# Kernel optimization log

Measured on AMD Instinct MI355X. Metric: run time of the kernel, lower is better.

The kernel has to match this reference:

```python
import jax, jax.numpy as jnp
import numpy as np

N = 100000      # hits
P = 512         # particle ids (0 = noise, skipped)
D = 8           # condensation-space dim
Q_MIN = 0.01
REPULSION_SCALING = 10.0


def setup_inputs() -> dict:
    key = jax.random.key(0)
    k1, k2, k3, k4, k5 = jax.random.split(key, 5)
    w = jax.random.normal(k1, (N,), dtype=jnp.float32)
    # beta in (0, 0.95) so arctanh stays well-conditioned
    beta = jax.random.uniform(k2, (N,), dtype=jnp.float32) * 0.95
    x = jax.random.normal(k3, (N, D), dtype=jnp.float32)
    y = jax.random.normal(k4, (N,), dtype=jnp.float32)
    particle_id = jax.random.randint(k5, (N,), 0, P)
    return {"w": w, "beta": beta, "x": x, "y": y, "particle_id": particle_id}


def _safe_sqrt(s):
    # sqrt with zero (sub)gradient at 0, matching torch.norm's behavior at 0
    pos = s > 0
    return jnp.where(pos, jnp.sqrt(jnp.where(pos, s, 1.0)), 0.0)


def _condensation_loss(beta, x, particle_id):
    n = beta.shape[0]
    q = jnp.arctanh(beta) ** 2 + Q_MIN                     # [N]
    # per-particle condensation point: hit with max q (torch.argmax -> first)
    q_max = jax.ops.segment_max(q, particle_id, num_segments=P)          # [P]
    counts = jax.ops.segment_sum(jnp.ones_like(q), particle_id, num_segments=P)
    is_max = q == q_max[particle_id]
    cand = jnp.where(is_max, jnp.arange(n), n)
    alpha_idx = jnp.clip(jax.ops.segment_min(cand, particle_id, num_segments=P), 0, n - 1)
    valid = (counts > 0) & (jnp.arange(P) != 0)            # skip noise pid 0 and absent pids
    q_alpha = jnp.where(valid, q_max, 0.0)                 # [P], sanitized (-inf for empty segs)
    x_alpha = x[alpha_idx]                                  # [P, D]
    # squared distances [N, P] via GEMM (avoids [N, P, D] intermediate)
    sq = (jnp.sum(x * x, axis=1, keepdims=True)
          - 2.0 * (x @ x_alpha.T)
          + jnp.sum(x_alpha * x_alpha, axis=1)[None, :])
    sq = jnp.maximum(sq, 0.0)
    dist = _safe_sqrt(sq)
    va = sq * q_alpha[None, :]                              # attractive potential
    vr = jnp.maximum(1.0 - dist, 0.0) * q_alpha[None, :]    # repulsive hinge
    M = (particle_id[:, None] == jnp.arange(P)[None, :]).astype(x.dtype)  # [N, P]
    per_p = jnp.mean(q[:, None] * (M * va + REPULSION_SCALING * (1.0 - M) * vr), axis=0)  # [P]
    return jnp.sum(jnp.where(valid, per_p, 0.0))


def reference(w, beta, x, y, particle_id):
    return _condensation_loss(beta, x, particle_id)
```

## Files before the change

### kernel.cpp

```cpp
#include <hip/hip_runtime.h>

#define P_IDS 512
#define DIM 8
#define QMIN 0.01f
#define REP 10.0f

typedef unsigned long long ull;
typedef float f32x4 __attribute__((ext_vector_type(4)));
typedef short s16x8 __attribute__((ext_vector_type(8)));

__device__ __forceinline__ unsigned int bf16_rne(float f) {
    unsigned int u = __float_as_uint(f);
    return (u + 0x7FFFu + ((u >> 16) & 1u)) >> 16;
}
__device__ __forceinline__ float bf16_to_f32(unsigned int h) {
    return __uint_as_float(h << 16);
}
__device__ __forceinline__ void split_pack(const float* v, uint4& hiw, uint4& low) {
    unsigned int hb[8], lb[8];
#pragma unroll
    for (int d = 0; d < 8; ++d) {
        unsigned int h = bf16_rne(v[d]);
        float rem = v[d] - bf16_to_f32(h);
        hb[d] = h;
        lb[d] = bf16_rne(rem);
    }
    hiw = make_uint4(hb[0] | (hb[1] << 16), hb[2] | (hb[3] << 16),
                     hb[4] | (hb[5] << 16), hb[6] | (hb[7] << 16));
    low = make_uint4(lb[0] | (lb[1] << 16), lb[2] | (lb[3] << 16),
                     lb[4] | (lb[5] << 16), lb[6] | (lb[7] << 16));
}

__launch_bounds__(256)
__global__ void stageA_kernel(const float* __restrict__ beta,
                              const int* __restrict__ pid,
                              float* __restrict__ q_out,
                              ull* __restrict__ tables,
                              int n) {
    __shared__ ull s_keys[P_IDS];
    s_keys[threadIdx.x] = 0ULL;
    s_keys[threadIdx.x + 256] = 0ULL;
    __syncthreads();
    int i = blockIdx.x * 256 + threadIdx.x;
    if (i < n) {
        float b = beta[i];
        float at = 0.5f * logf((1.0f + b) / (1.0f - b));
        float qv = fmaf(at, at, QMIN);
        q_out[i] = qv;
        ull key = ((ull)__float_as_uint(qv) << 32) |
                  (ull)(unsigned int)(~(unsigned int)i);
        atomicMax(&s_keys[pid[i]], key);
    }
    __syncthreads();
    ull* dst = tables + (size_t)blockIdx.x * P_IDS;
    dst[threadIdx.x] = s_keys[threadIdx.x];
    dst[threadIdx.x + 256] = s_keys[threadIdx.x + 256];
}

__launch_bounds__(64)
__global__ void stageB_kernel(const ull* __restrict__ tables, int ntab,
                              const float* __restrict__ x,
                              float2* __restrict__ meta,
                              float* __restrict__ x_alpha,
                              uint4* __restrict__ gB,
                              float* __restrict__ out) {
    int p = blockIdx.x;
    ull k = 0ULL;
    for (int t = threadIdx.x; t < ntab; t += 64) {
        ull v = tables[(size_t)t * P_IDS + p];
        k = (v > k) ? v : k;
    }
#pragma unroll
    for (int off = 32; off > 0; off >>= 1) {
        ull o = __shfl_down(k, off, 64);
        k = (o > k) ? o : k;
    }
    if (threadIdx.x == 0) {
        bool valid = (k != 0ULL) && (p != 0);
        float qa = valid ? __uint_as_float((unsigned int)(k >> 32)) : 0.0f;
        int idx = valid ? (int)(~(unsigned int)(k & 0xFFFFFFFFull)) : 0;
        float4 a = ((const float4*)x)[idx * 2];
        float4 b = ((const float4*)x)[idx * 2 + 1];
        float xa2 = a.x * a.x;
        xa2 = fmaf(a.y, a.y, xa2); xa2 = fmaf(a.z, a.z, xa2); xa2 = fmaf(a.w, a.w, xa2);
        xa2 = fmaf(b.x, b.x, xa2); xa2 = fmaf(b.y, b.y, xa2); xa2 = fmaf(b.z, b.z, xa2);
        xa2 = fmaf(b.w, b.w, xa2);
        ((float4*)x_alpha)[p * 2] = a;
        ((float4*)x_alpha)[p * 2 + 1] = b;
        meta[p] = make_float2(qa, xa2);
        float xv[8] = {a.x, a.y, a.z, a.w, b.x, b.y, b.z, b.w};
        uint4 hiw, low; split_pack(xv, hiw, low);
        gB[p] = hiw;
        gB[P_IDS + p] = low;
        if (p == 0) out[0] = 0.0f;
    }
}

__launch_bounds__(256)
__global__ void loss_kernel(const float* __restrict__ x,
                            const float* __restrict__ q,
                            const int* __restrict__ pid,
                            const float2* __restrict__ meta,
                            const float* __restrict__ x_alpha,
                            const uint4* __restrict__ gB,
                            float* __restrict__ out, int n) {
    __shared__ uint4  s_B[2 * P_IDS];
    __shared__ float2 s_meta[P_IDS];
    __shared__ uint4  s_A[128];
    __shared__ __align__(16) float s_xi2[64];
    __shared__ __align__(16) float s_qi[64];
    __shared__ __align__(16) int   s_pid[64];

    int tid = threadIdx.x;
    float partial = 0.0f;

    if (tid < 64) {
        int i = blockIdx.x * 64 + tid;
        bool act = i < n;
        int ii = act ? i : 0;
        float4 v0 = ((const float4*)x)[ii * 2];
        float4 v1 = ((const float4*)x)[ii * 2 + 1];
        float xv[8] = {v0.x, v0.y, v0.z, v0.w, v1.x, v1.y, v1.z, v1.w};
        float s = 0.0f;
#pragma unroll
        for (int d = 0; d < 8; ++d) s = fmaf(xv[d], xv[d], s);
        float qi = act ? q[ii] : 0.0f;
        int   pd = act ? pid[ii] : 0;
        s_xi2[tid] = act ? s : 0.0f;
        s_qi[tid]  = qi;
        s_pid[tid] = pd;
        float m2[8];
#pragma unroll
        for (int d = 0; d < 8; ++d) m2[d] = act ? (-2.0f * xv[d]) : 0.0f;
        uint4 hiw, low; split_pack(m2, hiw, low);
        s_A[tid] = hiw; s_A[64 + tid] = low;
        float2 mm = meta[pd];
        float4 a0 = ((const float4*)x_alpha)[pd * 2];
        float4 a1 = ((const float4*)x_alpha)[pd * 2 + 1];
        float dot = xv[0] * a0.x;
        dot = fmaf(xv[1], a0.y, dot); dot = fmaf(xv[2], a0.z, dot);
        dot = fmaf(xv[3], a0.w, dot); dot = fmaf(xv[4], a1.x, dot);
        dot = fmaf(xv[5], a1.y, dot); dot = fmaf(xv[6], a1.z, dot);
        dot = fmaf(xv[7], a1.w, dot);
        float sqe = fmaxf(fmaf(-2.0f, dot, s + mm.y), 0.0f);
        partial = qi * mm.x * sqe;
    }
    for (int k = tid; k < 2 * P_IDS; k += 256) s_B[k] = gB[k];
    for (int k = tid; k < P_IDS; k += 256) s_meta[k] = meta[k];
    __syncthreads();

    int lane = tid & 63;
    int wid  = tid >> 6;
    int grp  = lane >> 4;
    int col  = lane & 15;

    s16x8 av = *reinterpret_cast<const s16x8*>(
        &s_A[((grp & 1) << 6) + wid * 16 + col]);
    int rbase = wid * 16 + (grp << 2);
    f32x4 xi2r = *reinterpret_cast<const f32x4*>(&s_xi2[rbase]);
    f32x4 qir  = *reinterpret_cast<const f32x4*>(&s_qi[rbase]);
    int4  pidr = *reinterpret_cast<const int4*>(&s_pid[rbase]);

    const uint4* bptr = &s_B[((grp >= 2) ? P_IDS : 0) + col];
    f32x4 rp = {0.0f, 0.0f, 0.0f, 0.0f};

#pragma unroll
    for (int jt = 0; jt < P_IDS / 16; ++jt) {
        s16x8 bv = *reinterpret_cast<const s16x8*>(&bptr[jt * 16]);
        float2 mm = s_meta[jt * 16 + col];
        f32x4 c;
        c[0] = xi2r[0] + mm.y; c[1] = xi2r[1] + mm.y;
        c[2] = xi2r[2] + mm.y; c[3] = xi2r[3] + mm.y;
        c = __builtin_amdgcn_mfma_f32_16x16x32_bf16(av, bv, c, 0, 0, 0);
        float mn = fminf(fminf(c[0], c[1]), fminf(c[2], c[3]));
        if (__any(mn < 1.0f)) {
            int p = jt * 16 + col;
#pragma unroll
            for (int r = 0; r < 4; ++r) {
                float sq = fmaxf(c[r], 0.0f);
                float vr = fmaxf(1.0f - __builtin_amdgcn_sqrtf(sq), 0.0f);
                float w  = (pidr[r] == p) ? 0.0f : mm.x;
                rp[r] = fmaf(vr, w, rp[r]);
            }
        }
    }
    partial += REP * (qir[0] * rp[0] + qir[1] * rp[1] +
                      qir[2] * rp[2] + qir[3] * rp[3]);

#pragma unroll
    for (int off = 32; off > 0; off >>= 1)
        partial += __shfl_down(partial, off, 64);
    __shared__ float s_red[4];
    if ((tid & 63) == 0) s_red[tid >> 6] = partial;
    __syncthreads();
    if (tid == 0)
        atomicAdd(out, (s_red[0] + s_red[1] + s_red[2] + s_red[3]) / (float)n);
}

extern "C" void kernel_launch(void* const* d_in, const int* in_sizes, int n_in,
                              void* d_out, int out_size, void* d_ws, size_t ws_size,
                              hipStream_t stream) {
    int n = in_sizes[0];
    const float* beta = (const float*)d_in[1];
    const float* x    = (const float*)d_in[2];
    const int*   pid  = (const int*)d_in[4];
    float* out = (float*)d_out;

    int a_blocks = (n + 255) / 256;
    char* ws = (char*)d_ws;
    size_t tab_bytes = (size_t)a_blocks * P_IDS * sizeof(ull);
    tab_bytes = (tab_bytes + 255) & ~(size_t)255;
    size_t q_bytes = (((size_t)n * 4) + 255) & ~(size_t)255;
    ull*    tables  = (ull*)ws;
    float*  qbuf    = (float*)(ws + tab_bytes);
    char*   p0      = ws + tab_bytes + q_bytes;
    float2* meta    = (float2*)p0;
    float*  x_alpha = (float*)(p0 + P_IDS * sizeof(float2));
    uint4*  gB      = (uint4*)(p0 + P_IDS * sizeof(float2)
                                  + P_IDS * DIM * sizeof(float));

    stageA_kernel<<<a_blocks, 256, 0, stream>>>(beta, pid, qbuf, tables, n);
    stageB_kernel<<<P_IDS, 64, 0, stream>>>(tables, a_blocks, x, meta, x_alpha, gB, out);
    int loss_blocks = (n + 63) / 64;
    loss_kernel<<<loss_blocks, 256, 0, stream>>>(x, qbuf, pid, meta, x_alpha, gB, out, n);
}
```

Baseline: 102.5 us.

## Process 128 hits per loss block and transpose stage-A max tables

```diff
diff --git a/kernel.cpp b/kernel.cpp
--- a/kernel.cpp
+++ b/kernel.cpp
@@ -4,6 +4,7 @@
 #define DIM 8
 #define QMIN 0.01f
 #define REP 10.0f
+#define HITS_B 128
 
 typedef unsigned long long ull;
 typedef float f32x4 __attribute__((ext_vector_type(4)));
@@ -35,7 +36,7 @@
 __global__ void stageA_kernel(const float* __restrict__ beta,
                               const int* __restrict__ pid,
                               float* __restrict__ q_out,
-                              ull* __restrict__ tables,
+                              ull* __restrict__ tables, int ts,
                               int n) {
     __shared__ ull s_keys[P_IDS];
     s_keys[threadIdx.x] = 0ULL;
@@ -52,22 +53,22 @@
         atomicMax(&s_keys[pid[i]], key);
     }
     __syncthreads();
-    ull* dst = tables + (size_t)blockIdx.x * P_IDS;
-    dst[threadIdx.x] = s_keys[threadIdx.x];
-    dst[threadIdx.x + 256] = s_keys[threadIdx.x + 256];
+    tables[(size_t)threadIdx.x * ts + blockIdx.x] = s_keys[threadIdx.x];
+    tables[(size_t)(threadIdx.x + 256) * ts + blockIdx.x] = s_keys[threadIdx.x + 256];
 }
 
 __launch_bounds__(64)
-__global__ void stageB_kernel(const ull* __restrict__ tables, int ntab,
+__global__ void stageB_kernel(const ull* __restrict__ tables, int ts, int ntab,
                               const float* __restrict__ x,
                               float2* __restrict__ meta,
                               float* __restrict__ x_alpha,
                               uint4* __restrict__ gB,
                               float* __restrict__ out) {
     int p = blockIdx.x;
+    const ull* row = tables + (size_t)p * ts;
     ull k = 0ULL;
     for (int t = threadIdx.x; t < ntab; t += 64) {
-        ull v = tables[(size_t)t * P_IDS + p];
+        ull v = row[t];
         k = (v > k) ? v : k;
     }
 #pragma unroll
@@ -106,16 +107,16 @@
                             float* __restrict__ out, int n) {
     __shared__ uint4  s_B[2 * P_IDS];
     __shared__ float2 s_meta[P_IDS];
-    __shared__ uint4  s_A[128];
-    __shared__ __align__(16) float s_xi2[64];
-    __shared__ __align__(16) float s_qi[64];
-    __shared__ __align__(16) int   s_pid[64];
+    __shared__ uint4  s_A[2 * HITS_B];
+    __shared__ __align__(16) float s_xi2[HITS_B];
+    __shared__ __align__(16) float s_qi[HITS_B];
+    __shared__ __align__(16) int   s_pid[HITS_B];
 
     int tid = threadIdx.x;
     float partial = 0.0f;
 
-    if (tid < 64) {
-        int i = blockIdx.x * 64 + tid;
+    if (tid < HITS_B) {
+        int i = blockIdx.x * HITS_B + tid;
         bool act = i < n;
         int ii = act ? i : 0;
         float4 v0 = ((const float4*)x)[ii * 2];
@@ -133,7 +134,7 @@
 #pragma unroll
         for (int d = 0; d < 8; ++d) m2[d] = act ? (-2.0f * xv[d]) : 0.0f;
         uint4 hiw, low; split_pack(m2, hiw, low);
-        s_A[tid] = hiw; s_A[64 + tid] = low;
+        s_A[tid] = hiw; s_A[HITS_B + tid] = low;
         float2 mm = meta[pd];
         float4 a0 = ((const float4*)x_alpha)[pd * 2];
         float4 a1 = ((const float4*)x_alpha)[pd * 2 + 1];
@@ -150,42 +151,71 @@
     __syncthreads();
 
     int lane = tid & 63;
-    int wid  = tid >> 6;
+    int w    = tid >> 6;
     int grp  = lane >> 4;
     int col  = lane & 15;
-
-    s16x8 av = *reinterpret_cast<const s16x8*>(
-        &s_A[((grp & 1) << 6) + wid * 16 + col]);
-    int rbase = wid * 16 + (grp << 2);
-    f32x4 xi2r = *reinterpret_cast<const f32x4*>(&s_xi2[rbase]);
-    f32x4 qir  = *reinterpret_cast<const f32x4*>(&s_qi[rbase]);
-    int4  pidr = *reinterpret_cast<const int4*>(&s_pid[rbase]);
+    int hbase = w * 32;
+
+    s16x8 av0 = *reinterpret_cast<const s16x8*>(
+        &s_A[((grp & 1) ? HITS_B : 0) + hbase + col]);
+    s16x8 av1 = *reinterpret_cast<const s16x8*>(
+        &s_A[((grp & 1) ? HITS_B : 0) + hbase + 16 + col]);
+    int r0 = hbase + (grp << 2);
+    int r1 = hbase + 16 + (grp << 2);
+    f32x4 xi20 = *reinterpret_cast<const f32x4*>(&s_xi2[r0]);
+    f32x4 xi21 = *reinterpret_cast<const f32x4*>(&s_xi2[r1]);
+    f32x4 qi0  = *reinterpret_cast<const f32x4*>(&s_qi[r0]);
+    f32x4 qi1  = *reinterpret_cast<const f32x4*>(&s_qi[r1]);
+    int4  pd0  = *reinterpret_cast<const int4*>(&s_pid[r0]);
+    int4  pd1  = *reinterpret_cast<const int4*>(&s_pid[r1]);
 
     const uint4* bptr = &s_B[((grp >= 2) ? P_IDS : 0) + col];
-    f32x4 rp = {0.0f, 0.0f, 0.0f, 0.0f};
-
-#pragma unroll
+    f32x4 rp0 = {0.0f, 0.0f, 0.0f, 0.0f};
+    f32x4 rp1 = {0.0f, 0.0f, 0.0f, 0.0f};
+
+#pragma unroll 4
     for (int jt = 0; jt < P_IDS / 16; ++jt) {
         s16x8 bv = *reinterpret_cast<const s16x8*>(&bptr[jt * 16]);
         float2 mm = s_meta[jt * 16 + col];
-        f32x4 c;
-        c[0] = xi2r[0] + mm.y; c[1] = xi2r[1] + mm.y;
-        c[2] = xi2r[2] + mm.y; c[3] = xi2r[3] + mm.y;
-        c = __builtin_amdgcn_mfma_f32_16x16x32_bf16(av, bv, c, 0, 0, 0);
-        float mn = fminf(fminf(c[0], c[1]), fminf(c[2], c[3]));
-        if (__any(mn < 1.0f)) {
-            int p = jt * 16 + col;
+        int p = jt * 16 + col;
+        f32x4 c0, c1;
+        c0[0] = xi20[0] + mm.y; c0[1] = xi20[1] + mm.y;
+        c0[2] = xi20[2] + mm.y; c0[3] = xi20[3] + mm.y;
+        c1[0] = xi21[0] + mm.y; c1[1] = xi21[1] + mm.y;
+        c1[2] = xi21[2] + mm.y; c1[3] = xi21[3] + mm.y;
+        c0 = __builtin_amdgcn_mfma_f32_16x16x32_bf16(av0, bv, c0, 0, 0, 0);
+        c1 = __builtin_amdgcn_mfma_f32_16x16x32_bf16(av1, bv, c1, 0, 0, 0);
+        float mn0 = fminf(fminf(c0[0], c0[1]), fminf(c0[2], c0[3]));
+        if (__any(mn0 < 1.0f)) {
 #pragma unroll
             for (int r = 0; r < 4; ++r) {
-                float sq = fmaxf(c[r], 0.0f);
+                float sq = fmaxf(c0[r], 0.0f);
                 float vr = fmaxf(1.0f - __builtin_amdgcn_sqrtf(sq), 0.0f);
-                float w  = (pidr[r] == p) ? 0.0f : mm.x;
-                rp[r] = fmaf(vr, w, rp[r]);
+                float wgt = (pd0.x == p && r == 0) ? 0.0f :
+                            (pd0.y == p && r == 1) ? 0.0f :
+                            (pd0.z == p && r == 2) ? 0.0f :
+                            (pd0.w == p && r == 3) ? 0.0f : mm.x;
+                rp0[r] = fmaf(vr, wgt, rp0[r]);
             }
         }
-    }
-    partial += REP * (qir[0] * rp[0] + qir[1] * rp[1] +
-                      qir[2] * rp[2] + qir[3] * rp[3]);
+        float mn1 = fminf(fminf(c1[0], c1[1]), fminf(c1[2], c1[3]));
+        if (__any(mn1 < 1.0f)) {
+#pragma unroll
+            for (int r = 0; r < 4; ++r) {
+                float sq = fmaxf(c1[r], 0.0f);
+                float vr = fmaxf(1.0f - __builtin_amdgcn_sqrtf(sq), 0.0f);
+                float wgt = (pd1.x == p && r == 0) ? 0.0f :
+                            (pd1.y == p && r == 1) ? 0.0f :
+                            (pd1.z == p && r == 2) ? 0.0f :
+                            (pd1.w == p && r == 3) ? 0.0f : mm.x;
+                rp1[r] = fmaf(vr, wgt, rp1[r]);
+            }
+        }
+    }
+    partial += REP * (qi0[0] * rp0[0] + qi0[1] * rp0[1] +
+                      qi0[2] * rp0[2] + qi0[3] * rp0[3] +
+                      qi1[0] * rp1[0] + qi1[1] * rp1[1] +
+                      qi1[2] * rp1[2] + qi1[3] * rp1[3]);
 
 #pragma unroll
     for (int off = 32; off > 0; off >>= 1)
@@ -207,8 +237,9 @@
     float* out = (float*)d_out;
 
     int a_blocks = (n + 255) / 256;
+    int ts = (a_blocks + 7) & ~7;
     char* ws = (char*)d_ws;
-    size_t tab_bytes = (size_t)a_blocks * P_IDS * sizeof(ull);
+    size_t tab_bytes = (size_t)P_IDS * ts * sizeof(ull);
     tab_bytes = (tab_bytes + 255) & ~(size_t)255;
     size_t q_bytes = (((size_t)n * 4) + 255) & ~(size_t)255;
     ull*    tables  = (ull*)ws;
@@ -219,8 +250,8 @@
     uint4*  gB      = (uint4*)(p0 + P_IDS * sizeof(float2)
                                   + P_IDS * DIM * sizeof(float));
 
-    stageA_kernel<<<a_blocks, 256, 0, stream>>>(beta, pid, qbuf, tables, n);
-    stageB_kernel<<<P_IDS, 64, 0, stream>>>(tables, a_blocks, x, meta, x_alpha, gB, out);
-    int loss_blocks = (n + 63) / 64;
+    stageA_kernel<<<a_blocks, 256, 0, stream>>>(beta, pid, qbuf, tables, ts, n);
+    stageB_kernel<<<P_IDS, 64, 0, stream>>>(tables, ts, a_blocks, x, meta, x_alpha, gB, out);
+    int loss_blocks = (n + HITS_B - 1) / HITS_B;
     loss_kernel<<<loss_blocks, 256, 0, stream>>>(x, qbuf, pid, meta, x_alpha, gB, out, n);
 }
```

Result: faster. 89.48 us (-12.7%).
